# Performance work log

Measured on AMD Instinct MI355X. Metric: run time of the kernel, lower is better.

Reference implementation:

```python
import jax, jax.numpy as jnp
import numpy as np


def _conv3x3(x, w):
    # x: [N,C,H,W], w: [O,I,3,3], stride 1, padding 1 -> SAME
    return jax.lax.conv_general_dilated(
        x, w, window_strides=(1, 1), padding='SAME',
        dimension_numbers=('NCHW', 'OIHW', 'NCHW'))


def setup_inputs() -> dict:
    key = jax.random.key(0)
    k1, k2, k3, k4 = jax.random.split(key, 4)
    # He-like init scale for 3x3 convs
    x = jax.random.normal(k1, (8, 1, 512, 512), dtype=jnp.float32)
    w1 = jax.random.normal(k2, (8, 1, 3, 3), dtype=jnp.float32) * (2.0 / (1 * 9)) ** 0.5
    wmid = jax.random.normal(k3, (18, 8, 8, 3, 3), dtype=jnp.float32) * (2.0 / (8 * 9)) ** 0.5
    w20 = jax.random.normal(k4, (1, 8, 3, 3), dtype=jnp.float32) * (2.0 / (8 * 9)) ** 0.5
    return {'x': x, 'w1': w1, 'wmid': wmid, 'w20': w20}


def reference(x, w1, wmid, w20):
    y = jax.nn.relu(_conv3x3(x, w1))  # conv1 + relu
    # conv2..conv19: 18 identical 8->8 conv+relu layers, scanned over stacked weights
    def body(y, w):
        return jax.nn.relu(_conv3x3(y, w)), None
    y, _ = jax.lax.scan(body, y, wmid)
    return _conv3x3(y, w20)  # conv20, no relu
```

## Files before the change

### kernel.cpp

```cpp
#include <hip/hip_runtime.h>

typedef _Float16 f16;
typedef _Float16 f16x8 __attribute__((ext_vector_type(8)));
typedef _Float16 f16x4 __attribute__((ext_vector_type(4)));
typedef float v4f __attribute__((ext_vector_type(4)));

constexpr int H = 512, W = 512, NB = 8;
constexpr int ROWS = 514;
constexpr int COLS = 528;
constexpr int CH = 8;
constexpr size_t ROWBYTES = (size_t)COLS * CH * 2;
constexpr size_t PLANE_ELEMS = (size_t)ROWS * COLS * CH;
constexpr size_t PLANE_BYTES = PLANE_ELEMS * 2;

constexpr int RSP = 145;
constexpr int RSPC = RSP * CH;
constexpr int LDS_ROWB = RSP * 16;
constexpr int WTAB_L = 3072;

constexpr int FRSP = 81;
constexpr int FRSPC = FRSP * CH;
constexpr int FROWB = FRSP * 16;
constexpr int INR = 12;
constexpr int ARR = 10;

__device__ __forceinline__ void gload_lds16(const void* g, void* l) {
    __builtin_amdgcn_global_load_lds(
        (const __attribute__((address_space(1))) unsigned int*)g,
        (__attribute__((address_space(3))) unsigned int*)l, 16, 0, 0);
}
__device__ __forceinline__ void gload_lds4(const void* g, void* l) {
    __builtin_amdgcn_global_load_lds(
        (const __attribute__((address_space(1))) unsigned int*)g,
        (__attribute__((address_space(3))) unsigned int*)l, 4, 0, 0);
}

__global__ void zero_borders(f16* __restrict__ base, size_t set_stride) {
    const int i = blockIdx.x * 256 + threadIdx.x;
    if (i >= 9248) return;
    const int img = blockIdx.y, set = blockIdx.z;
    int row, col;
    if (i < 1056) { row = (i < 528) ? 0 : 513; col = (i < 528) ? i : i - 528; }
    else {
        const int j = i - 1056;
        row = 1 + (j >> 4);
        const int c4 = j & 15;
        col = (c4 < 8) ? c4 : 512 + c4;
    }
    f16x8 z = {};
    f16* p = base + (size_t)set * set_stride + ((size_t)img * ROWS + row) * COLS * CH + (size_t)col * CH;
    *(f16x8*)p = z;
}

__global__ void build_wtab(const float* __restrict__ wmid,
                           const float* __restrict__ w20,
                           f16* __restrict__ wtab) {
    const int l = blockIdx.x;
    const int lane = threadIdx.x;
    const float* wt = (l < 18) ? wmid + (size_t)l * 576 : w20;
    const int COUT = (l < 18) ? 8 : 1;
    const int n = lane & 15, q = lane >> 4;
#pragma unroll
    for (int g = 0; g < 3; ++g) {
        const int t = g * 4 + q;
        f16x8 hv, lv;
#pragma unroll
        for (int j = 0; j < 8; ++j) {
            float wv = 0.f;
            if (n < 8) {
                if (t <= 8 && n < COUT) wv = wt[(n * 8 + j) * 9 + t];
            } else {
                const int o = n - 8;
                if (t >= 3 && o < COUT) wv = wt[(o * 8 + j) * 9 + (t - 3)];
            }
            const f16 h = (f16)wv;
            hv[j] = h;
            lv[j] = (f16)(wv - (float)h);
        }
        f16* dst = wtab + (size_t)l * WTAB_L + (g * 2) * 512 + lane * 8;
        *(f16x8*)dst = hv;
        *(f16x8*)(dst + 512) = lv;
    }
}

__global__ __launch_bounds__(256) void conv1_kernel(
    const float* __restrict__ in, const float* __restrict__ wt,
    f16* __restrict__ out)
{
    const int x0 = (blockIdx.x * 64 + threadIdx.x) * 4;
    const int y  = blockIdx.y * 4 + threadIdx.y;
    const int b  = blockIdx.z;
    const float* inb = in + (size_t)b * H * W;

    float patch[3][6];
#pragma unroll
    for (int r = 0; r < 3; ++r) {
        const int iy = y - 1 + r;
        if (iy >= 0 && iy < H) {
            const float* rp = inb + (size_t)iy * W;
            const float4 v = *(const float4*)(rp + x0);
            patch[r][1] = v.x; patch[r][2] = v.y; patch[r][3] = v.z; patch[r][4] = v.w;
            patch[r][0] = (x0 > 0)     ? rp[x0 - 1] : 0.f;
            patch[r][5] = (x0 + 4 < W) ? rp[x0 + 4] : 0.f;
        } else {
#pragma unroll
            for (int k = 0; k < 6; ++k) patch[r][k] = 0.f;
        }
    }

    float acc[8][4];
#pragma unroll
    for (int o = 0; o < 8; ++o) {
        const float* wo = wt + o * 9;
        float a0 = 0.f, a1 = 0.f, a2 = 0.f, a3 = 0.f;
#pragma unroll
        for (int r = 0; r < 3; ++r)
#pragma unroll
            for (int k = 0; k < 3; ++k) {
                const float wv = wo[r * 3 + k];
                a0 = fmaf(wv, patch[r][k + 0], a0);
                a1 = fmaf(wv, patch[r][k + 1], a1);
                a2 = fmaf(wv, patch[r][k + 2], a2);
                a3 = fmaf(wv, patch[r][k + 3], a3);
            }
        acc[o][0] = a0; acc[o][1] = a1; acc[o][2] = a2; acc[o][3] = a3;
    }

#pragma unroll
    for (int j = 0; j < 4; ++j) {
        f16x8 hv;
#pragma unroll
        for (int o = 0; o < 8; ++o)
            hv[o] = (f16)fmaxf(acc[o][j], 0.f);
        const size_t off = (((size_t)b * ROWS + (y + 1)) * COLS + (x0 + j + 8)) * CH;
        *(f16x8*)(out + off) = hv;
    }
}

__global__ __launch_bounds__(256, 4) void conv2fused(
    const f16* __restrict__ in,
    const f16* __restrict__ wtA, const f16* __restrict__ wtB,
    f16* __restrict__ outp)
{
    __shared__ __align__(16) f16 aring[ARR * FRSPC];
    __shared__ __align__(16) f16 inring[INR * FRSPC];

    const int wave = threadIdx.x >> 6, lane = threadIdx.x & 63;
    const int img = blockIdx.x, xt = blockIdx.y;
    const int x0 = xt * 64;
    const int base = blockIdx.z * 32;

    f16x8 ahiW[3], aloW[3], bhiW[3], bloW[3];
#pragma unroll
    for (int g = 0; g < 3; ++g) {
        const f16* wa = wtA + (g * 2) * 512 + lane * 8;
        ahiW[g] = *(const f16x8*)wa;  aloW[g] = *(const f16x8*)(wa + 512);
        const f16* wb = wtB + (g * 2) * 512 + lane * 8;
        bhiW[g] = *(const f16x8*)wb;  bloW[g] = *(const f16x8*)(wb + 512);
    }

    const char* src = (const char*)in + (size_t)img * PLANE_BYTES + (size_t)x0 * 16;

    auto stage = [&](int r0, int cnt) {
        for (int rr = wave; rr < cnt; rr += 4) {
            const int row = r0 + rr;
            const int rowc = min(max(row, 0), 513);
            const int slot = ((row % INR) + INR) % INR;
            const char* gs = src + (size_t)rowc * ROWBYTES;
            char* ld = (char*)inring + slot * FROWB;
            gload_lds16(gs + lane * 16, ld);
            if (lane < 16) gload_lds16(gs + 1024 + lane * 16, ld + 1024);
        }
    };

    const int n = lane & 15, q = lane >> 4;
    int tyv[3], txv[3];
#pragma unroll
    for (int g = 0; g < 3; ++g) { const int t = g * 4 + q; tyv[g] = t / 3 - 1; txv[g] = t % 3 - 1; }
    const int rowoff = q >> 1, choff = (q & 1) * 4;
    const bool xe0 = (xt == 0), xe7 = (xt == 7);

    auto computeA = [&](int rA) {
        int irow[3];
#pragma unroll
        for (int g = 0; g < 3; ++g) {
            const int r = rA + tyv[g];
            irow[g] = (((r % INR) + INR) % INR) * FRSPC;
        }
        const int gyA = rA + rowoff;
        const int wrow = (gyA % ARR) * FRSPC;
        const bool zr = (gyA == 0) || (gyA == 513);
#pragma unroll
        for (int s = 0; s < 5; ++s) {
            v4f acc = {0.f,0.f,0.f,0.f}, acc2 = {0.f,0.f,0.f,0.f};
#pragma unroll
            for (int g = 0; g < 3; ++g) {
                const f16x8 xv = *(const f16x8*)&inring[irow[g] + (16 * s + n + txv[g]) * CH];
                acc  = __builtin_amdgcn_mfma_f32_16x16x32_f16(ahiW[g], xv, acc,  0, 0, 0);
                acc2 = __builtin_amdgcn_mfma_f32_16x16x32_f16(aloW[g], xv, acc2, 0, 0, 0);
            }
            const v4f res = acc + acc2;
            f16x4 hv;
#pragma unroll
            for (int c = 0; c < 4; ++c) hv[c] = (f16)fmaxf(res[c], 0.f);
            if (zr || (xe0 && s == 0 && n == 7) || (xe7 && s == 4 && n == 8)) {
                hv[0] = (f16)0.f; hv[1] = (f16)0.f; hv[2] = (f16)0.f; hv[3] = (f16)0.f;
            }
            *(f16x4*)&aring[wrow + (16 * s + n) * CH + choff] = hv;
        }
    };

    auto computeB = [&](int rB) {
        int brow[3];
#pragma unroll
        for (int g = 0; g < 3; ++g) brow[g] = ((rB + tyv[g]) % ARR) * FRSPC;
        const int gyB = rB + rowoff;
        f16* orow = outp + ((size_t)img * ROWS + gyB) * COLS * CH + (size_t)(x0 + 8) * CH + choff;
#pragma unroll
        for (int s = 0; s < 4; ++s) {
            v4f acc = {0.f,0.f,0.f,0.f}, acc2 = {0.f,0.f,0.f,0.f};
#pragma unroll
            for (int g = 0; g < 3; ++g) {
                const f16x8 xv = *(const f16x8*)&aring[brow[g] + (16 * s + n + txv[g] + 8) * CH];
                acc  = __builtin_amdgcn_mfma_f32_16x16x32_f16(bhiW[g], xv, acc,  0, 0, 0);
                acc2 = __builtin_amdgcn_mfma_f32_16x16x32_f16(bloW[g], xv, acc2, 0, 0, 0);
            }
            const v4f res = acc + acc2;
            f16x4 hv;
#pragma unroll
            for (int c = 0; c < 4; ++c) hv[c] = (f16)fmaxf(res[c], 0.f);
            *(f16x4*)(orow + (size_t)(16 * s + n) * CH) = hv;
        }
    };

    stage(base - 1, 12);
    __syncthreads();
    if (wave == 0) computeA(base);

    for (int t = 0; t < 4; ++t) {
        computeA(base + 8 * t + 2 + 2 * wave);
        __syncthreads();
        if (t < 3) stage(base + 8 * t + 11, 8);
        computeB(base + 8 * t + 1 + 2 * wave);
        __syncthreads();
    }
}

template<bool RELU, bool FINAL>
__global__ __launch_bounds__(256) void convmfma(
    const f16* __restrict__ in, const f16* __restrict__ wtab_l,
    f16* __restrict__ outp, float* __restrict__ out_final)
{
    __shared__ __align__(16) f16 lds[2][10 * RSPC];

    const int wave = threadIdx.x >> 6, lane = threadIdx.x & 63;
    const int img = blockIdx.x;
    const int x0 = blockIdx.y * 128;
    const int ybase = blockIdx.z * 32;

    f16x8 bhi[3], blo[3];
#pragma unroll
    for (int g = 0; g < 3; ++g) {
        const f16* wp = wtab_l + (g * 2) * 512 + lane * 8;
        bhi[g] = *(const f16x8*)wp;
        blo[g] = *(const f16x8*)(wp + 512);
    }

    const char* src = (const char*)in + (size_t)img * PLANE_BYTES + (size_t)x0 * 16;
    auto stage = [&](int buf, int y0) {
        char* dst = (char*)&lds[buf][0];
        for (int qq = wave; qq < 30; qq += 4) {
            const int r = qq / 3, c = qq % 3;
            const char* gs = src + (size_t)(y0 + r) * ROWBYTES;
            char* ld = dst + r * LDS_ROWB;
            if (c < 2) gload_lds16(gs + c * 1024 + lane * 16, ld + c * 1024);
            else       gload_lds4(gs + 2048 + lane * 4, ld + 2048);
        }
    };

    const int n = lane & 15, q = lane >> 4, m = lane & 15;
    int abase[3];
#pragma unroll
    for (int g = 0; g < 3; ++g) {
        const int t = g * 4 + q;
        const int ty = t / 3 - 1, tx = t % 3 - 1;
        abase[g] = (2 * wave + ty + 1) * RSP + (m + tx + 8);
    }
    const int rowoff = q >> 1;
    const int choff = (q & 1) * 4;

    stage(0, ybase);
    __syncthreads();

    for (int t = 0; t < 4; ++t) {
        if (t < 3) stage((t + 1) & 1, ybase + 8 * (t + 1));
        const f16* L = &lds[t & 1][0];
        const int Y = ybase + 8 * t + 2 * wave;
#pragma unroll
        for (int s = 0; s < 8; ++s) {
            v4f acc = {0.f,0.f,0.f,0.f}, acc2 = {0.f,0.f,0.f,0.f};
#pragma unroll
            for (int g = 0; g < 3; ++g) {
                const f16x8 xv = *(const f16x8*)&L[(abase[g] + 16 * s) * CH];
                acc  = __builtin_amdgcn_mfma_f32_16x16x32_f16(bhi[g], xv, acc,  0, 0, 0);
                acc2 = __builtin_amdgcn_mfma_f32_16x16x32_f16(blo[g], xv, acc2, 0, 0, 0);
            }
            const v4f res = acc + acc2;
            if constexpr (!FINAL) {
                f16x4 hv;
#pragma unroll
                for (int c = 0; c < 4; ++c) {
                    float v = res[c];
                    if (RELU) v = fmaxf(v, 0.f);
                    hv[c] = (f16)v;
                }
                const int gy = Y + rowoff + 1;
                const int gx = x0 + 16 * s + n + 8;
                *(f16x4*)(outp + ((size_t)img * ROWS + gy) * COLS * CH + (size_t)gx * CH + choff) = hv;
            } else {
                if ((q & 1) == 0) {
                    const int gy = Y + rowoff, gx = x0 + 16 * s + n;
                    out_final[((size_t)img * H + gy) * W + gx] = res[0];
                }
            }
        }
        if (t < 3) __syncthreads();
    }
}

extern "C" void kernel_launch(void* const* d_in, const int* in_sizes, int n_in,
                              void* d_out, int out_size, void* d_ws, size_t ws_size,
                              hipStream_t stream) {
    const float* x    = (const float*)d_in[0];
    const float* w1   = (const float*)d_in[1];
    const float* wmid = (const float*)d_in[2];
    const float* w20  = (const float*)d_in[3];
    float* out = (float*)d_out;

    const size_t wtab_bytes = (size_t)19 * WTAB_L * 2;
    int g = NB;
    while (g > 1 && 2 * (size_t)g * PLANE_BYTES + wtab_bytes > ws_size) g >>= 1;

    f16* act0 = (f16*)d_ws;
    f16* act1 = act0 + (size_t)g * PLANE_ELEMS;
    f16* wtab = act1 + (size_t)g * PLANE_ELEMS;

    zero_borders<<<dim3(37, g, 2), 256, 0, stream>>>(act0, (size_t)g * PLANE_ELEMS);
    build_wtab<<<19, 64, 0, stream>>>(wmid, w20, wtab);

    for (int b0 = 0; b0 < NB; b0 += g) {
        conv1_kernel<<<dim3(2, 128, g), dim3(64, 4), 0, stream>>>(
            x + (size_t)b0 * H * W, w1, act0);
        for (int k = 0; k < 9; ++k) {
            const f16* s0 = (k & 1) ? act1 : act0;
            f16*       d0 = (k & 1) ? act0 : act1;
            conv2fused<<<dim3(g, 8, 16), 256, 0, stream>>>(
                s0, wtab + (size_t)(2 * k) * WTAB_L, wtab + (size_t)(2 * k + 1) * WTAB_L, d0);
        }
        convmfma<false, true><<<dim3(g, 4, 16), 256, 0, stream>>>(
            act1, wtab + (size_t)18 * WTAB_L, nullptr, out + (size_t)b0 * H * W);
    }
}
```

Measured before the change: 270.9 us.

## Fuse three mid conv layers per kernel instead of two

Replaces the two-layer fused conv kernel with a three-layer one. It keeps intermediate activations in two LDS ring buffers and pipelines stages A, B and C across row tiles. The number of mid-layer launches drops from 9 to 6, which cuts global activation round trips by a third. In exchange there is more halo recomputation, larger LDS use that limits occupancy to 3 blocks, and fewer blocks (12 row chunks of uneven 40/48 size) per launch.

New measurement: 281.3 us. 1.04x slower.

```diff
diff --git a/kernel.cpp b/kernel.cpp
--- a/kernel.cpp
+++ b/kernel.cpp
@@ -21,8 +21,13 @@
 constexpr int FRSP = 81;
 constexpr int FRSPC = FRSP * CH;
 constexpr int FROWB = FRSP * 16;
-constexpr int INR = 12;
+constexpr int INR = 14;
 constexpr int ARR = 10;
+constexpr int BRR = 10;
+
+__device__ __forceinline__ int ringmod(int a, int m) {
+    int r = a % m; return (r < 0) ? r + m : r;
+}
 
 __device__ __forceinline__ void gload_lds16(const void* g, void* l) {
     __builtin_amdgcn_global_load_lds(
@@ -137,26 +142,32 @@
     }
 }
 
-__global__ __launch_bounds__(256, 4) void conv2fused(
+__global__ __launch_bounds__(256, 3) void conv3fused(
     const f16* __restrict__ in,
-    const f16* __restrict__ wtA, const f16* __restrict__ wtB,
+    const f16* __restrict__ wtA, const f16* __restrict__ wtB, const f16* __restrict__ wtC,
     f16* __restrict__ outp)
 {
-    __shared__ __align__(16) f16 aring[ARR * FRSPC];
-    __shared__ __align__(16) f16 inring[INR * FRSPC];
+    __shared__ __align__(16) f16 shmem[8 + (ARR + BRR + INR) * FRSPC];
+    f16* aring  = shmem + 8;
+    f16* bring  = aring + ARR * FRSPC;
+    f16* inring = bring + BRR * FRSPC;
 
     const int wave = threadIdx.x >> 6, lane = threadIdx.x & 63;
     const int img = blockIdx.x, xt = blockIdx.y;
     const int x0 = xt * 64;
-    const int base = blockIdx.z * 32;
-
-    f16x8 ahiW[3], aloW[3], bhiW[3], bloW[3];
+    const int cz = blockIdx.z;
+    const int base = (cz < 8) ? cz * 40 : 320 + (cz - 8) * 48;
+    const int nt   = (cz < 8) ? 5 : 6;
+
+    f16x8 whiA[3], wloA[3], whiB[3], wloB[3], whiC[3], wloC[3];
 #pragma unroll
     for (int g = 0; g < 3; ++g) {
         const f16* wa = wtA + (g * 2) * 512 + lane * 8;
-        ahiW[g] = *(const f16x8*)wa;  aloW[g] = *(const f16x8*)(wa + 512);
+        whiA[g] = *(const f16x8*)wa;  wloA[g] = *(const f16x8*)(wa + 512);
         const f16* wb = wtB + (g * 2) * 512 + lane * 8;
-        bhiW[g] = *(const f16x8*)wb;  bloW[g] = *(const f16x8*)(wb + 512);
+        whiB[g] = *(const f16x8*)wb;  wloB[g] = *(const f16x8*)(wb + 512);
+        const f16* wc = wtC + (g * 2) * 512 + lane * 8;
+        whiC[g] = *(const f16x8*)wc;  wloC[g] = *(const f16x8*)(wc + 512);
     }
 
     const char* src = (const char*)in + (size_t)img * PLANE_BYTES + (size_t)x0 * 16;
@@ -165,7 +176,7 @@
         for (int rr = wave; rr < cnt; rr += 4) {
             const int row = r0 + rr;
             const int rowc = min(max(row, 0), 513);
-            const int slot = ((row % INR) + INR) % INR;
+            const int slot = ringmod(row, INR);
             const char* gs = src + (size_t)rowc * ROWBYTES;
             char* ld = (char*)inring + slot * FROWB;
             gload_lds16(gs + lane * 16, ld);
@@ -183,21 +194,18 @@
     auto computeA = [&](int rA) {
         int irow[3];
 #pragma unroll
-        for (int g = 0; g < 3; ++g) {
-            const int r = rA + tyv[g];
-            irow[g] = (((r % INR) + INR) % INR) * FRSPC;
-        }
+        for (int g = 0; g < 3; ++g) irow[g] = ringmod(rA + tyv[g], INR) * FRSPC;
         const int gyA = rA + rowoff;
-        const int wrow = (gyA % ARR) * FRSPC;
-        const bool zr = (gyA == 0) || (gyA == 513);
+        const int wrow = ringmod(gyA, ARR) * FRSPC;
+        const bool zr = (gyA <= 0) || (gyA >= 513);
 #pragma unroll
         for (int s = 0; s < 5; ++s) {
             v4f acc = {0.f,0.f,0.f,0.f}, acc2 = {0.f,0.f,0.f,0.f};
 #pragma unroll
             for (int g = 0; g < 3; ++g) {
                 const f16x8 xv = *(const f16x8*)&inring[irow[g] + (16 * s + n + txv[g]) * CH];
-                acc  = __builtin_amdgcn_mfma_f32_16x16x32_f16(ahiW[g], xv, acc,  0, 0, 0);
-                acc2 = __builtin_amdgcn_mfma_f32_16x16x32_f16(aloW[g], xv, acc2, 0, 0, 0);
+                acc  = __builtin_amdgcn_mfma_f32_16x16x32_f16(whiA[g], xv, acc,  0, 0, 0);
+                acc2 = __builtin_amdgcn_mfma_f32_16x16x32_f16(wloA[g], xv, acc2, 0, 0, 0);
             }
             const v4f res = acc + acc2;
             f16x4 hv;
@@ -211,19 +219,46 @@
     };
 
     auto computeB = [&](int rB) {
+        int arow[3];
+#pragma unroll
+        for (int g = 0; g < 3; ++g) arow[g] = ringmod(rB + tyv[g], ARR) * FRSPC;
+        const int gyB = rB + rowoff;
+        const int wrow = ringmod(gyB, BRR) * FRSPC;
+        const bool zr = (gyB <= 0) || (gyB >= 513);
+#pragma unroll
+        for (int s = 0; s < 5; ++s) {
+            v4f acc = {0.f,0.f,0.f,0.f}, acc2 = {0.f,0.f,0.f,0.f};
+#pragma unroll
+            for (int g = 0; g < 3; ++g) {
+                const f16x8 xv = *(const f16x8*)&aring[arow[g] + (16 * s + n + txv[g]) * CH];
+                acc  = __builtin_amdgcn_mfma_f32_16x16x32_f16(whiB[g], xv, acc,  0, 0, 0);
+                acc2 = __builtin_amdgcn_mfma_f32_16x16x32_f16(wloB[g], xv, acc2, 0, 0, 0);
+            }
+            const v4f res = acc + acc2;
+            f16x4 hv;
+#pragma unroll
+            for (int c = 0; c < 4; ++c) hv[c] = (f16)fmaxf(res[c], 0.f);
+            if (zr || (xe0 && s == 0 && n == 7) || (xe7 && s == 4 && n == 8)) {
+                hv[0] = (f16)0.f; hv[1] = (f16)0.f; hv[2] = (f16)0.f; hv[3] = (f16)0.f;
+            }
+            *(f16x4*)&bring[wrow + (16 * s + n) * CH + choff] = hv;
+        }
+    };
+
+    auto computeC = [&](int rC) {
         int brow[3];
 #pragma unroll
-        for (int g = 0; g < 3; ++g) brow[g] = ((rB + tyv[g]) % ARR) * FRSPC;
-        const int gyB = rB + rowoff;
-        f16* orow = outp + ((size_t)img * ROWS + gyB) * COLS * CH + (size_t)(x0 + 8) * CH + choff;
+        for (int g = 0; g < 3; ++g) brow[g] = ringmod(rC + tyv[g], BRR) * FRSPC;
+        const int gyC = rC + rowoff;
+        f16* orow = outp + ((size_t)img * ROWS + gyC) * COLS * CH + (size_t)(x0 + 8) * CH + choff;
 #pragma unroll
         for (int s = 0; s < 4; ++s) {
             v4f acc = {0.f,0.f,0.f,0.f}, acc2 = {0.f,0.f,0.f,0.f};
 #pragma unroll
             for (int g = 0; g < 3; ++g) {
-                const f16x8 xv = *(const f16x8*)&aring[brow[g] + (16 * s + n + txv[g] + 8) * CH];
-                acc  = __builtin_amdgcn_mfma_f32_16x16x32_f16(bhiW[g], xv, acc,  0, 0, 0);
-                acc2 = __builtin_amdgcn_mfma_f32_16x16x32_f16(bloW[g], xv, acc2, 0, 0, 0);
+                const f16x8 xv = *(const f16x8*)&bring[brow[g] + (16 * s + n + 8 + txv[g]) * CH];
+                acc  = __builtin_amdgcn_mfma_f32_16x16x32_f16(whiC[g], xv, acc,  0, 0, 0);
+                acc2 = __builtin_amdgcn_mfma_f32_16x16x32_f16(wloC[g], xv, acc2, 0, 0, 0);
             }
             const v4f res = acc + acc2;
             f16x4 hv;
@@ -233,17 +268,22 @@
         }
     };
 
-    stage(base - 1, 12);
+    stage(base - 2, 14);
     __syncthreads();
-    if (wave == 0) computeA(base);
-
-    for (int t = 0; t < 4; ++t) {
-        computeA(base + 8 * t + 2 + 2 * wave);
+    if (wave < 2) computeA(base - 1 + 2 * wave);
+    __syncthreads();
+    if (wave == 0) computeB(base);
+    __syncthreads();
+
+    for (int t = 0; t < nt; ++t) {
+        computeA(base + 8 * t + 3 + 2 * wave);
+        if (t > 0) computeC(base + 8 * (t - 1) + 1 + 2 * wave);
         __syncthreads();
-        if (t < 3) stage(base + 8 * t + 11, 8);
-        computeB(base + 8 * t + 1 + 2 * wave);
+        if (t < nt - 1) stage(base + 8 * t + 12, 8);
+        computeB(base + 8 * t + 2 + 2 * wave);
         __syncthreads();
     }
+    computeC(base + 8 * (nt - 1) + 1 + 2 * wave);
 }
 
 template<bool RELU, bool FINAL>
@@ -351,13 +391,17 @@
     for (int b0 = 0; b0 < NB; b0 += g) {
         conv1_kernel<<<dim3(2, 128, g), dim3(64, 4), 0, stream>>>(
             x + (size_t)b0 * H * W, w1, act0);
-        for (int k = 0; k < 9; ++k) {
+        for (int k = 0; k < 6; ++k) {
             const f16* s0 = (k & 1) ? act1 : act0;
             f16*       d0 = (k & 1) ? act0 : act1;
-            conv2fused<<<dim3(g, 8, 16), 256, 0, stream>>>(
-                s0, wtab + (size_t)(2 * k) * WTAB_L, wtab + (size_t)(2 * k + 1) * WTAB_L, d0);
+            conv3fused<<<dim3(g, 8, 12), 256, 0, stream>>>(
+                s0,
+                wtab + (size_t)(3 * k + 0) * WTAB_L,
+                wtab + (size_t)(3 * k + 1) * WTAB_L,
+                wtab + (size_t)(3 * k + 2) * WTAB_L,
+                d0);
         }
         convmfma<false, true><<<dim3(g, 4, 16), 256, 0, stream>>>(
-            act1, wtab + (size_t)18 * WTAB_L, nullptr, out + (size_t)b0 * H * W);
-    }
-}
+            act0, wtab + (size_t)18 * WTAB_L, nullptr, out + (size_t)b0 * H * W);
+    }
+}
```

## Split intermediate LDS ring into channel half-planes and prefetch input rows earlier

Applied to the files above, without the earlier changes.

Stores the fused kernel's intermediate activation ring as two separate 4-channel planes instead of interleaved 8-channel rows, and reads them back as two 8-byte loads. The aim is to cut LDS bank conflicts on the 8-byte writes and 16-byte reads. The input ring grows from 12 to 14 rows so half of the next row block can be staged before computeA and half after, overlapping global-to-LDS copies with compute at the cost of an extra barrier. In the other conv kernel, the 4-byte global-to-LDS tail loads become 16-byte loads on 16 lanes.

New measurement: 280.5 us. 3.6% more time.

```diff
diff --git a/kernel.cpp b/kernel.cpp
--- a/kernel.cpp
+++ b/kernel.cpp
@@ -21,18 +21,18 @@
 constexpr int FRSP = 81;
 constexpr int FRSPC = FRSP * CH;
 constexpr int FROWB = FRSP * 16;
-constexpr int INR = 12;
+constexpr int INR = 14;
 constexpr int ARR = 10;
+constexpr int APL = ARR * FRSP * 4;
+
+__device__ __forceinline__ int ringmod(int a, int m) {
+    int r = a % m; return (r < 0) ? r + m : r;
+}
 
 __device__ __forceinline__ void gload_lds16(const void* g, void* l) {
     __builtin_amdgcn_global_load_lds(
         (const __attribute__((address_space(1))) unsigned int*)g,
         (__attribute__((address_space(3))) unsigned int*)l, 16, 0, 0);
-}
-__device__ __forceinline__ void gload_lds4(const void* g, void* l) {
-    __builtin_amdgcn_global_load_lds(
-        (const __attribute__((address_space(1))) unsigned int*)g,
-        (__attribute__((address_space(3))) unsigned int*)l, 4, 0, 0);
 }
 
 __global__ void zero_borders(f16* __restrict__ base, size_t set_stride) {
@@ -142,8 +142,9 @@
     const f16* __restrict__ wtA, const f16* __restrict__ wtB,
     f16* __restrict__ outp)
 {
-    __shared__ __align__(16) f16 aring[ARR * FRSPC];
-    __shared__ __align__(16) f16 inring[INR * FRSPC];
+    __shared__ __align__(16) f16 shmem[2 * APL + INR * FRSPC];
+    f16* aring  = shmem;
+    f16* inring = shmem + 2 * APL;
 
     const int wave = threadIdx.x >> 6, lane = threadIdx.x & 63;
     const int img = blockIdx.x, xt = blockIdx.y;
@@ -165,7 +166,7 @@
         for (int rr = wave; rr < cnt; rr += 4) {
             const int row = r0 + rr;
             const int rowc = min(max(row, 0), 513);
-            const int slot = ((row % INR) + INR) % INR;
+            const int slot = ringmod(row, INR);
             const char* gs = src + (size_t)rowc * ROWBYTES;
             char* ld = (char*)inring + slot * FROWB;
             gload_lds16(gs + lane * 16, ld);
@@ -177,18 +178,16 @@
     int tyv[3], txv[3];
 #pragma unroll
     for (int g = 0; g < 3; ++g) { const int t = g * 4 + q; tyv[g] = t / 3 - 1; txv[g] = t % 3 - 1; }
-    const int rowoff = q >> 1, choff = (q & 1) * 4;
+    const int rowoff = q >> 1;
+    const int hplane = (q & 1);
     const bool xe0 = (xt == 0), xe7 = (xt == 7);
 
     auto computeA = [&](int rA) {
         int irow[3];
 #pragma unroll
-        for (int g = 0; g < 3; ++g) {
-            const int r = rA + tyv[g];
-            irow[g] = (((r % INR) + INR) % INR) * FRSPC;
-        }
+        for (int g = 0; g < 3; ++g) irow[g] = ringmod(rA + tyv[g], INR) * FRSPC;
         const int gyA = rA + rowoff;
-        const int wrow = (gyA % ARR) * FRSPC;
+        const int wrow = ringmod(gyA, ARR) * FRSP;
         const bool zr = (gyA == 0) || (gyA == 513);
 #pragma unroll
         for (int s = 0; s < 5; ++s) {
@@ -206,22 +205,26 @@
             if (zr || (xe0 && s == 0 && n == 7) || (xe7 && s == 4 && n == 8)) {
                 hv[0] = (f16)0.f; hv[1] = (f16)0.f; hv[2] = (f16)0.f; hv[3] = (f16)0.f;
             }
-            *(f16x4*)&aring[wrow + (16 * s + n) * CH + choff] = hv;
+            *(f16x4*)&aring[hplane * APL + (wrow + 16 * s + n) * 4] = hv;
         }
     };
 
     auto computeB = [&](int rB) {
         int brow[3];
 #pragma unroll
-        for (int g = 0; g < 3; ++g) brow[g] = ((rB + tyv[g]) % ARR) * FRSPC;
+        for (int g = 0; g < 3; ++g) brow[g] = ringmod(rB + tyv[g], ARR) * FRSP;
         const int gyB = rB + rowoff;
-        f16* orow = outp + ((size_t)img * ROWS + gyB) * COLS * CH + (size_t)(x0 + 8) * CH + choff;
+        f16* orow = outp + ((size_t)img * ROWS + gyB) * COLS * CH
+                  + (size_t)(x0 + 8) * CH + hplane * 4;
 #pragma unroll
         for (int s = 0; s < 4; ++s) {
             v4f acc = {0.f,0.f,0.f,0.f}, acc2 = {0.f,0.f,0.f,0.f};
 #pragma unroll
             for (int g = 0; g < 3; ++g) {
-                const f16x8 xv = *(const f16x8*)&aring[brow[g] + (16 * s + n + txv[g] + 8) * CH];
+                const int p = (brow[g] + 16 * s + n + 8 + txv[g]) * 4;
+                const f16x4 xl = *(const f16x4*)&aring[p];
+                const f16x4 xh = *(const f16x4*)&aring[p + APL];
+                const f16x8 xv = __builtin_shufflevector(xl, xh, 0, 1, 2, 3, 4, 5, 6, 7);
                 acc  = __builtin_amdgcn_mfma_f32_16x16x32_f16(bhiW[g], xv, acc,  0, 0, 0);
                 acc2 = __builtin_amdgcn_mfma_f32_16x16x32_f16(bloW[g], xv, acc2, 0, 0, 0);
             }
@@ -236,11 +239,13 @@
     stage(base - 1, 12);
     __syncthreads();
     if (wave == 0) computeA(base);
+    __syncthreads();
 
     for (int t = 0; t < 4; ++t) {
+        if (t < 3) stage(base + 8 * t + 11, 4);
         computeA(base + 8 * t + 2 + 2 * wave);
         __syncthreads();
-        if (t < 3) stage(base + 8 * t + 11, 8);
+        if (t < 3) stage(base + 8 * t + 15, 4);
         computeB(base + 8 * t + 1 + 2 * wave);
         __syncthreads();
     }
@@ -274,7 +279,7 @@
             const char* gs = src + (size_t)(y0 + r) * ROWBYTES;
             char* ld = dst + r * LDS_ROWB;
             if (c < 2) gload_lds16(gs + c * 1024 + lane * 16, ld + c * 1024);
-            else       gload_lds4(gs + 2048 + lane * 4, ld + 2048);
+            else if (lane < 16) gload_lds16(gs + 2048 + lane * 16, ld + 2048);
         }
     };
 
```
